# Kernel tuning notes

Hardware: AMD Instinct MI355X
Metric: run time of the kernel (lower is better)

## Reference

```python
import jax, jax.numpy as jnp
import numpy as np

H = 512      # hidden_size
V = 50257    # output_size (vocab)
M = 200      # memory_size
B = 64       # batch


def setup_inputs() -> dict:
    key = jax.random.key(0)
    ks = jax.random.split(key, 24)
    s = 1.0 / np.sqrt(H)
    f32 = jnp.float32
    return {
        "rmn_hidden": jax.random.normal(ks[0], (1, B, H), f32),
        "cell": jax.random.normal(ks[1], (1, B, H), f32),
        "context": jax.random.normal(ks[2], (1, B, H), f32),
        # embedding tables
        "emb": jax.random.normal(ks[3], (V, H), f32) * 0.02,
        "m_emb": jax.random.normal(ks[4], (V, H), f32) * 0.02,
        "c_emb": jax.random.normal(ks[5], (V, H), f32) * 0.02,
        # LSTMCell(2H -> H), torch gate order i, f, g, o
        "lstm_W_ih": jax.random.normal(ks[6], (4 * H, 2 * H), f32) * s,
        "lstm_W_hh": jax.random.normal(ks[7], (4 * H, H), f32) * s,
        "lstm_b_ih": jax.random.normal(ks[8], (4 * H,), f32) * s,
        "lstm_b_hh": jax.random.normal(ks[9], (4 * H,), f32) * s,
        # GRUCell(H -> H), torch gate order r, z, n
        "gru_W_ih": jax.random.normal(ks[10], (3 * H, H), f32) * s,
        "gru_W_hh": jax.random.normal(ks[11], (3 * H, H), f32) * s,
        "gru_b_ih": jax.random.normal(ks[12], (3 * H,), f32) * s,
        "gru_b_hh": jax.random.normal(ks[13], (3 * H,), f32) * s,
        # mb_attn_linear(M -> M)
        "attn_W": jax.random.normal(ks[14], (M, M), f32) * (1.0 / np.sqrt(M)),
        "attn_b": jax.random.normal(ks[15], (M,), f32) * (1.0 / np.sqrt(M)),
        # out Linear(2H -> V)
        "out_W": jax.random.normal(ks[16], (V, 2 * H), f32) * (1.0 / np.sqrt(2 * H)),
        "out_b": jax.random.normal(ks[17], (V,), f32) * (1.0 / np.sqrt(2 * H)),
        # int inputs
        "input_ids": jax.random.randint(ks[18], (1, B), 0, V, jnp.int32),
        "memory_tensor": jax.random.randint(ks[19], (M, B), 0, V, jnp.int32),
        "batch_size": B,
        "memory_size": M,
    }


def reference(rmn_hidden, cell, context, emb, m_emb, c_emb,
              lstm_W_ih, lstm_W_hh, lstm_b_ih, lstm_b_hh,
              gru_W_ih, gru_W_hh, gru_b_ih, gru_b_hh,
              attn_W, attn_b, out_W, out_b,
              input_ids, memory_tensor, batch_size, memory_size):
    sig = jax.nn.sigmoid
    h = rmn_hidden.shape[-1]
    # embedding + relu, concat with context along feature dim
    x = jax.nn.relu(emb[input_ids])                       # (1, B, H)
    ctx = context.reshape(1, batch_size, h)               # (1, B, H)
    xc = jnp.concatenate([x, ctx], axis=2)[0]             # (B, 2H)
    h0, c0 = rmn_hidden[0], cell[0]                       # (B, H)
    # LSTMCell
    gates = xc @ lstm_W_ih.T + lstm_b_ih + h0 @ lstm_W_hh.T + lstm_b_hh
    i, f, g, o = jnp.split(gates, 4, axis=-1)
    c1 = sig(f) * c0 + sig(i) * jnp.tanh(g)
    h1 = sig(o) * jnp.tanh(c1)                            # lstm_hidden (B, H)
    # memory attention
    in_mem = m_emb[memory_tensor]                         # (M, B, H)
    out_mem = c_emb[memory_tensor]                        # (M, B, H)
    attn = jnp.einsum('mbh,bh->bm', in_mem, h1)           # (B, M)
    attn = attn @ attn_W.T + attn_b
    # NOTE: original applies nn.LogSoftmax here (not Softmax) -- faithful.
    attn_dist = jax.nn.log_softmax(attn, axis=-1)         # (B, M)
    memory_context = jnp.einsum('mbh,bm->bh', out_mem, attn_dist)  # (B, H)
    # GRUCell(memory_context, h1)
    gi = memory_context @ gru_W_ih.T + gru_b_ih
    gh = h1 @ gru_W_hh.T + gru_b_hh
    gi_r, gi_z, gi_n = jnp.split(gi, 3, axis=-1)
    gh_r, gh_z, gh_n = jnp.split(gh, 3, axis=-1)
    r = sig(gi_r + gh_r)
    z = sig(gi_z + gh_z)
    n = jnp.tanh(gi_n + r * gh_n)
    mb = (1.0 - z) * n + z * h1                           # (B, H)
    # output projection + log-softmax
    mbc = jnp.concatenate([mb[None], ctx], axis=2)[0]     # (B, 2H)
    output = jax.nn.log_softmax(mbc @ out_W.T + out_b, axis=-1)  # (B, V)
    return (output, h1, c1[None])
```

## Files before the change

### kernel.cpp

```cpp
#include <hip/hip_runtime.h>
#include <math.h>

#define B 64
#define H 512
#define V 50257
#define M 200
#define H2 1024
#define H3 1536
#define H4 2048
#define NB2 1571

typedef short short8 __attribute__((ext_vector_type(8)));
typedef float f32x4 __attribute__((ext_vector_type(4)));

__device__ __forceinline__ float sigf(float x) { return 1.f / (1.f + expf(-x)); }

__device__ __forceinline__ short bf16c(float f) {
  unsigned u = __builtin_bit_cast(unsigned, f);
  unsigned r = u + 0x7fffu + ((u >> 16) & 1u);
  return (short)(r >> 16);
}

__device__ __forceinline__ short8 cvt8(float4 a, float4 b) {
  short8 w;
  w[0] = bf16c(a.x); w[1] = bf16c(a.y); w[2] = bf16c(a.z); w[3] = bf16c(a.w);
  w[4] = bf16c(b.x); w[5] = bf16c(b.y); w[6] = bf16c(b.z); w[7] = bf16c(b.w);
  return w;
}

__global__ __launch_bounds__(256) void k_build_A(
    const float* __restrict__ emb, const float* __restrict__ ctx,
    const float* __restrict__ h0, const int* __restrict__ ids,
    short* __restrict__ A) {
  int k = blockIdx.x * 256 + threadIdx.x;
  int b = blockIdx.y;
  float v;
  if (k < 512) {
    v = emb[(size_t)ids[b] * H + k];
    v = v > 0.f ? v : 0.f;
  } else if (k < 1024) {
    v = ctx[b * H + (k - 512)];
  } else {
    v = h0[b * H + (k - 1024)];
  }
  A[b * H3 + k] = bf16c(v);
}

__global__ __launch_bounds__(256) void k_lstm_gates_mfma(
    const short* __restrict__ A, const float* __restrict__ W_ih,
    const float* __restrict__ W_hh, const float* __restrict__ b_ih,
    const float* __restrict__ b_hh, float* __restrict__ gates) {
  __shared__ float sred[3][64][16];
  const int tid = threadIdx.x;
  const int lane = tid & 63, wid = tid >> 6;
  const int col = lane & 15, g = lane >> 4;
  const int j = blockIdx.x * 16 + col;
  const int kbase = wid * 384;

  f32x4 acc[4];
  #pragma unroll
  for (int t = 0; t < 4; ++t) acc[t] = (f32x4)(0.f);

  #pragma unroll 2
  for (int it = 0; it < 12; ++it) {
    int k0 = kbase + it * 32;
    const float* wp;
    if (k0 < 1024) wp = W_ih + (size_t)j * H2 + k0 + g * 8;
    else           wp = W_hh + (size_t)j * H + (k0 - 1024) + g * 8;
    float4 wa = *(const float4*)wp;
    float4 wb = *(const float4*)(wp + 4);
    short8 bf = cvt8(wa, wb);
    #pragma unroll
    for (int t = 0; t < 4; ++t) {
      short8 af = *(const short8*)(A + (size_t)(col + t * 16) * H3 + k0 + g * 8);
      acc[t] = __builtin_amdgcn_mfma_f32_16x16x32_bf16(af, bf, acc[t], 0, 0, 0);
    }
  }

  if (wid) {
    #pragma unroll
    for (int t = 0; t < 4; ++t)
      #pragma unroll
      for (int r = 0; r < 4; ++r) sred[wid - 1][lane][t * 4 + r] = acc[t][r];
  }
  __syncthreads();
  if (wid == 0) {
    float bias = b_ih[j] + b_hh[j];
    #pragma unroll
    for (int t = 0; t < 4; ++t)
      #pragma unroll
      for (int r = 0; r < 4; ++r) {
        float s = acc[t][r] + sred[0][lane][t * 4 + r] + sred[1][lane][t * 4 + r] +
                  sred[2][lane][t * 4 + r];
        int brow = t * 16 + g * 4 + r;
        gates[brow * H4 + j] = s + bias;
      }
  }
}

__global__ __launch_bounds__(256) void k_lstm_cell(
    const float* __restrict__ gates, const float* __restrict__ c0,
    float* __restrict__ h1, float* __restrict__ c1, short* __restrict__ h1bf) {
  int idx = blockIdx.x * 256 + threadIdx.x;
  int b = idx >> 9, h = idx & 511;
  const float* g = gates + b * H4;
  float gi = g[h], gf = g[H + h], gg = g[2 * H + h], go = g[3 * H + h];
  float c = sigf(gf) * c0[idx] + sigf(gi) * tanhf(gg);
  c1[idx] = c;
  float hv = sigf(go) * tanhf(c);
  h1[idx] = hv;
  h1bf[idx] = bf16c(hv);
}

__global__ __launch_bounds__(256) void k_attn_scores(
    const float* __restrict__ m_emb, const int* __restrict__ mt,
    const float* __restrict__ h1, float* __restrict__ attn) {
  int wave = (blockIdx.x * 256 + threadIdx.x) >> 6;
  int lane = threadIdx.x & 63;
  int m = wave >> 6, b = wave & 63;
  int row = mt[m * B + b];
  const float4* e = (const float4*)(m_emb + (size_t)row * H);
  const float4* hv = (const float4*)(h1 + b * H);
  float4 a0 = e[lane], a1 = e[64 + lane];
  float4 b0 = hv[lane], b1 = hv[64 + lane];
  float acc = a0.x * b0.x + a0.y * b0.y + a0.z * b0.z + a0.w * b0.w +
              a1.x * b1.x + a1.y * b1.y + a1.z * b1.z + a1.w * b1.w;
  for (int off = 32; off > 0; off >>= 1) acc += __shfl_down(acc, off);
  if (lane == 0) attn[b * M + m] = acc;
}

__global__ __launch_bounds__(256) void k_attn_lin_lsm(
    const float* __restrict__ attn, const float* __restrict__ attn_W,
    const float* __restrict__ attn_b, float* __restrict__ attn_d) {
  __shared__ float arow[M];
  __shared__ float vals[256];
  __shared__ float red[256];
  int b = blockIdx.x, tid = threadIdx.x;
  if (tid < M) arow[tid] = attn[b * M + tid];
  __syncthreads();
  float v = -1e30f;
  if (tid < M) {
    const float* w = attn_W + tid * M;
    float a0 = attn_b[tid], a1 = 0.f;
    for (int m = 0; m < M; m += 2) {
      a0 = fmaf(arow[m], w[m], a0);
      a1 = fmaf(arow[m + 1], w[m + 1], a1);
    }
    v = a0 + a1;
  }
  vals[tid] = v;
  red[tid] = v;
  __syncthreads();
  for (int off = 128; off > 0; off >>= 1) {
    if (tid < off) red[tid] = fmaxf(red[tid], red[tid + off]);
    __syncthreads();
  }
  float mx = red[0];
  __syncthreads();
  red[tid] = (tid < M) ? expf(vals[tid] - mx) : 0.f;
  __syncthreads();
  for (int off = 128; off > 0; off >>= 1) {
    if (tid < off) red[tid] += red[tid + off];
    __syncthreads();
  }
  float lse = mx + logf(red[0]);
  if (tid < M) attn_d[b * M + tid] = vals[tid] - lse;
}

__global__ __launch_bounds__(256) void k_mem_ctx_partial(
    const float* __restrict__ c_emb, const int* __restrict__ mt,
    const float* __restrict__ attn_d, float* __restrict__ mcp) {
  int b = blockIdx.x;
  int chunk = blockIdx.y;
  int tid = threadIdx.x;
  __shared__ int rows[50];
  __shared__ float w[50];
  if (tid < 50) {
    int m = chunk * 50 + tid;
    rows[tid] = mt[m * B + b];
    w[tid] = attn_d[b * M + m];
  }
  __syncthreads();
  float acc0 = 0.f, acc1 = 0.f;
  #pragma unroll 5
  for (int i = 0; i < 50; ++i) {
    const float* e = c_emb + (size_t)rows[i] * H;
    acc0 = fmaf(w[i], e[tid], acc0);
    acc1 = fmaf(w[i], e[256 + tid], acc1);
  }
  mcp[(chunk * B + b) * H + tid] = acc0;
  mcp[(chunk * B + b) * H + 256 + tid] = acc1;
}

__global__ __launch_bounds__(256) void k_mem_ctx_reduce(
    const float* __restrict__ mcp, short* __restrict__ mcbf) {
  int idx = blockIdx.x * 256 + threadIdx.x;
  float s = 0.f;
  for (int c = 0; c < 4; ++c) s += mcp[c * (B * H) + idx];
  mcbf[idx] = bf16c(s);
}

__global__ __launch_bounds__(256) void k_gru_gates_mfma(
    const short* __restrict__ mcbf, const short* __restrict__ h1bf,
    const float* __restrict__ W_ih, const float* __restrict__ W_hh,
    const float* __restrict__ b_ih, const float* __restrict__ b_hh,
    float* __restrict__ gi, float* __restrict__ gh) {
  __shared__ float sred[3][64][16];
  const int tid = threadIdx.x;
  const int lane = tid & 63, wid = tid >> 6;
  const int col = lane & 15, g = lane >> 4;
  const int half = blockIdx.x / 96;
  const int j = (blockIdx.x % 96) * 16 + col;
  const short* A = half ? h1bf : mcbf;
  const float* W = half ? W_hh : W_ih;
  const float* bias = half ? b_hh : b_ih;
  float* out = half ? gh : gi;
  const int kbase = wid * 128;

  f32x4 acc[4];
  #pragma unroll
  for (int t = 0; t < 4; ++t) acc[t] = (f32x4)(0.f);

  #pragma unroll
  for (int it = 0; it < 4; ++it) {
    int k0 = kbase + it * 32;
    const float* wp = W + (size_t)j * H + k0 + g * 8;
    float4 wa = *(const float4*)wp;
    float4 wb = *(const float4*)(wp + 4);
    short8 bf = cvt8(wa, wb);
    #pragma unroll
    for (int t = 0; t < 4; ++t) {
      short8 af = *(const short8*)(A + (size_t)(col + t * 16) * H + k0 + g * 8);
      acc[t] = __builtin_amdgcn_mfma_f32_16x16x32_bf16(af, bf, acc[t], 0, 0, 0);
    }
  }

  if (wid) {
    #pragma unroll
    for (int t = 0; t < 4; ++t)
      #pragma unroll
      for (int r = 0; r < 4; ++r) sred[wid - 1][lane][t * 4 + r] = acc[t][r];
  }
  __syncthreads();
  if (wid == 0) {
    float bv = bias[j];
    #pragma unroll
    for (int t = 0; t < 4; ++t)
      #pragma unroll
      for (int r = 0; r < 4; ++r) {
        float s = acc[t][r] + sred[0][lane][t * 4 + r] + sred[1][lane][t * 4 + r] +
                  sred[2][lane][t * 4 + r];
        int brow = t * 16 + g * 4 + r;
        out[brow * H3 + j] = s + bv;
      }
  }
}

__global__ __launch_bounds__(256) void k_gru_combine(
    const float* __restrict__ gi, const float* __restrict__ gh,
    const float* __restrict__ h1, const float* __restrict__ ctx,
    short* __restrict__ Abf) {
  int idx = blockIdx.x * 256 + threadIdx.x;
  int b = idx >> 9, h = idx & 511;
  const float* gib = gi + b * H3;
  const float* ghb = gh + b * H3;
  float r = sigf(gib[h] + ghb[h]);
  float z = sigf(gib[H + h] + ghb[H + h]);
  float n = tanhf(gib[2 * H + h] + r * ghb[2 * H + h]);
  float mb = (1.f - z) * n + z * h1[idx];
  Abf[b * H2 + h] = bf16c(mb);
  Abf[b * H2 + H + h] = bf16c(ctx[idx]);
}

__global__ __launch_bounds__(256) void k_out_gemm_mfma(
    const short* __restrict__ Abf, const float* __restrict__ W,
    const float* __restrict__ bias, float* __restrict__ out,
    float* __restrict__ pm, float* __restrict__ ps) {
  __shared__ short8 Wl[512];
  __shared__ float spm[4][32];
  __shared__ float sps[4][32];
  const int tid = threadIdx.x;
  const int lane = tid & 63, wid = tid >> 6;
  const int v0 = blockIdx.x * 32;

  const int sr = tid >> 3, sj = tid & 7;
  const int sidx = sr * 8 + (sj ^ (sr & 7));
  int vr = v0 + sr; if (vr >= V) vr = V - 1;
  const float* wsrc = W + (size_t)vr * H2 + sj * 8;

  const int col = lane & 15, g = lane >> 4;
  const int ct = wid & 1, bh = wid >> 1;
  const int wrow = ct * 16 + col;
  const short* a0p = Abf + (size_t)(bh * 32 + col) * H2 + g * 8;
  const short* a1p = a0p + 16 * H2;

  f32x4 acc0 = (f32x4)(0.f), acc1 = (f32x4)(0.f);

  {
    float4 wa = *(const float4*)(wsrc);
    float4 wb = *(const float4*)(wsrc + 4);
    Wl[sidx] = cvt8(wa, wb);
  }
  __syncthreads();

  int cur = 0;
  for (int kt = 0; kt < 16; ++kt) {
    float4 nwa, nwb;
    if (kt < 15) {
      nwa = *(const float4*)(wsrc + (kt + 1) * 64);
      nwb = *(const float4*)(wsrc + (kt + 1) * 64 + 4);
    }
    {
      const short8* Wb = Wl + cur * 256;
      #pragma unroll
      for (int kw = 0; kw < 2; ++kw) {
        int c = kw * 4 + g;
        short8 bf  = Wb[wrow * 8 + (c ^ (wrow & 7))];
        short8 af0 = *(const short8*)(a0p + kt * 64 + kw * 32);
        short8 af1 = *(const short8*)(a1p + kt * 64 + kw * 32);
        acc0 = __builtin_amdgcn_mfma_f32_16x16x32_bf16(af0, bf, acc0, 0, 0, 0);
        acc1 = __builtin_amdgcn_mfma_f32_16x16x32_bf16(af1, bf, acc1, 0, 0, 0);
      }
    }
    if (kt < 15) {
      Wl[(cur ^ 1) * 256 + sidx] = cvt8(nwa, nwb);
      __syncthreads();
      cur ^= 1;
    }
  }

  const int v = v0 + ct * 16 + col;
  const float bv = (v < V) ? bias[v] : 0.f;
  #pragma unroll
  for (int ai = 0; ai < 2; ++ai) {
    f32x4 a = ai ? acc1 : acc0;
    #pragma unroll
    for (int r = 0; r < 4; ++r) {
      int b = bh * 32 + ai * 16 + g * 4 + r;
      float x = a[r] + bv;
      if (v < V) out[(size_t)b * V + v] = x;
      float xm = (v < V) ? x : -1e30f;
      float mx = xm;
      #pragma unroll
      for (int off = 1; off < 16; off <<= 1) mx = fmaxf(mx, __shfl_xor(mx, off));
      float e = (v < V) ? expf(xm - mx) : 0.f;
      #pragma unroll
      for (int off = 1; off < 16; off <<= 1) e += __shfl_xor(e, off);
      if (col == 0) {
        spm[wid][ai * 16 + g * 4 + r] = mx;
        sps[wid][ai * 16 + g * 4 + r] = e;
      }
    }
  }
  __syncthreads();
  if (tid < 64) {
    int b = tid;
    int w0 = (b >> 5) * 2;
    int bl = b & 31;
    float m1 = spm[w0][bl],     s1 = sps[w0][bl];
    float m2 = spm[w0 + 1][bl], s2 = sps[w0 + 1][bl];
    float nm = fmaxf(m1, m2);
    float s = s1 * expf(m1 - nm) + s2 * expf(m2 - nm);
    pm[(size_t)b * NB2 + blockIdx.x] = nm;
    ps[(size_t)b * NB2 + blockIdx.x] = s;
  }
}

__global__ __launch_bounds__(256) void k_lsm_finalize(
    const float* __restrict__ pm, const float* __restrict__ ps,
    float* __restrict__ lse) {
  int b = blockIdx.x, tid = threadIdx.x;
  float m = -1e30f, s = 0.f;
  for (int gq = tid; gq < NB2; gq += 256) {
    float m2 = pm[(size_t)b * NB2 + gq], s2 = ps[(size_t)b * NB2 + gq];
    float nm = fmaxf(m, m2);
    s = s * expf(m - nm) + s2 * expf(m2 - nm);
    m = nm;
  }
  __shared__ float sm[256], ss[256];
  sm[tid] = m; ss[tid] = s;
  __syncthreads();
  for (int off = 128; off > 0; off >>= 1) {
    if (tid < off) {
      float m1 = sm[tid], s1 = ss[tid];
      float m2 = sm[tid + off], s2 = ss[tid + off];
      float nm = fmaxf(m1, m2);
      sm[tid] = nm;
      ss[tid] = s1 * expf(m1 - nm) + s2 * expf(m2 - nm);
    }
    __syncthreads();
  }
  if (tid == 0) lse[b] = sm[0] + logf(ss[0]);
}

__global__ __launch_bounds__(256) void k_lsm_apply(
    float* __restrict__ out, const float* __restrict__ lse) {
  int b = blockIdx.y, tid = threadIdx.x;
  float l = lse[b];
  int v = blockIdx.x * 1024 + tid * 4;
  float* row = out + (size_t)b * V;
  if (v + 3 < V) {
    float4 x = *(const float4*)(row + v);
    x.x -= l; x.y -= l; x.z -= l; x.w -= l;
    *(float4*)(row + v) = x;
  } else {
    for (int i = 0; i < 4 && v + i < V; ++i) row[v + i] -= l;
  }
}

extern "C" void kernel_launch(void* const* d_in, const int* in_sizes, int n_in,
                              void* d_out, int out_size, void* d_ws, size_t ws_size,
                              hipStream_t stream) {
  const float* h0    = (const float*)d_in[0];
  const float* c0    = (const float*)d_in[1];
  const float* ctx   = (const float*)d_in[2];
  const float* emb   = (const float*)d_in[3];
  const float* m_emb = (const float*)d_in[4];
  const float* c_emb = (const float*)d_in[5];
  const float* lWih  = (const float*)d_in[6];
  const float* lWhh  = (const float*)d_in[7];
  const float* lbih  = (const float*)d_in[8];
  const float* lbhh  = (const float*)d_in[9];
  const float* gWih  = (const float*)d_in[10];
  const float* gWhh  = (const float*)d_in[11];
  const float* gbih  = (const float*)d_in[12];
  const float* gbhh  = (const float*)d_in[13];
  const float* aW    = (const float*)d_in[14];
  const float* ab    = (const float*)d_in[15];
  const float* oW    = (const float*)d_in[16];
  const float* ob    = (const float*)d_in[17];
  const int* ids     = (const int*)d_in[18];
  const int* mt      = (const int*)d_in[19];

  float* out = (float*)d_out;
  float* h1  = out + (size_t)B * V;
  float* c1  = h1 + B * H;

  float* ws    = (float*)d_ws;
  short* Albf  = (short*)ws;
  float* gates = ws + 49152;
  short* h1bf  = (short*)(gates + B * H4);
  float* attn  = gates + B * H4 + 16384;
  float* attnd = attn + B * M;
  float* mcp   = attnd + B * M;
  short* mcbf  = (short*)(mcp + 4 * B * H);
  float* gi    = mcp + 4 * B * H + 16384;
  float* gh    = gi + B * H3;
  short* Abf   = (short*)(gh + B * H3);
  float* pm    = gh + B * H3 + 32768;
  float* ps    = pm + (size_t)B * NB2;
  float* lse   = ps + (size_t)B * NB2;

  dim3 g1(6, B);
  k_build_A<<<g1, 256, 0, stream>>>(emb, ctx, h0, ids, Albf);
  k_lstm_gates_mfma<<<128, 256, 0, stream>>>(Albf, lWih, lWhh, lbih, lbhh, gates);
  k_lstm_cell<<<(B * H) / 256, 256, 0, stream>>>(gates, c0, h1, c1, h1bf);
  k_attn_scores<<<(M * B) / 4, 256, 0, stream>>>(m_emb, mt, h1, attn);
  k_attn_lin_lsm<<<B, 256, 0, stream>>>(attn, aW, ab, attnd);
  dim3 g6(B, 4);
  k_mem_ctx_partial<<<g6, 256, 0, stream>>>(c_emb, mt, attnd, mcp);
  k_mem_ctx_reduce<<<(B * H) / 256, 256, 0, stream>>>(mcp, mcbf);
  k_gru_gates_mfma<<<192, 256, 0, stream>>>(mcbf, h1bf, gWih, gWhh, gbih, gbhh, gi, gh);
  k_gru_combine<<<(B * H) / 256, 256, 0, stream>>>(gi, gh, h1, ctx, Abf);
  k_out_gemm_mfma<<<NB2, 256, 0, stream>>>(Abf, oW, ob, out, pm, ps);
  k_lsm_finalize<<<B, 256, 0, stream>>>(pm, ps, lse);
  dim3 g11(50, B);
  k_lsm_apply<<<g11, 256, 0, stream>>>(out, lse);
}
```

Baseline: 137.3 us.

## Widen output GEMM tile to 64 vocab rows and stage activations in LDS

The output projection kernel now computes 64 vocab rows per block instead of 32, halving the block count. Each wave computes a 32x32 tile with four MFMA accumulators, so every A and W fragment is reused twice. The bf16 activation matrix is also staged through swizzled, double-buffered shared memory rather than read from global memory by each wave. This cuts repeated activation loads and the number of partial log-softmax entries, at the cost of more LDS and registers per block and fewer blocks to spread across CUs.

```diff
diff --git a/kernel.cpp b/kernel.cpp
--- a/kernel.cpp
+++ b/kernel.cpp
@@ -8,7 +8,7 @@
 #define H2 1024
 #define H3 1536
 #define H4 2048
-#define NB2 1571
+#define NB 786
 
 typedef short short8 __attribute__((ext_vector_type(8)));
 typedef float f32x4 __attribute__((ext_vector_type(4)));
@@ -276,78 +276,110 @@
     const short* __restrict__ Abf, const float* __restrict__ W,
     const float* __restrict__ bias, float* __restrict__ out,
     float* __restrict__ pm, float* __restrict__ ps) {
-  __shared__ short8 Wl[512];
+  __shared__ short8 Wl[1024];
+  __shared__ short8 Al[1024];
   __shared__ float spm[4][32];
   __shared__ float sps[4][32];
   const int tid = threadIdx.x;
   const int lane = tid & 63, wid = tid >> 6;
-  const int v0 = blockIdx.x * 32;
-
-  const int sr = tid >> 3, sj = tid & 7;
-  const int sidx = sr * 8 + (sj ^ (sr & 7));
+  const int v0 = blockIdx.x * 64;
+
+  const int sr = tid >> 2, sj = tid & 3;
+  const int sx = sr & 7;
+  const int sidx0 = sr * 8 + ((2 * sj) ^ sx);
+  const int sidx1 = sr * 8 + ((2 * sj + 1) ^ sx);
   int vr = v0 + sr; if (vr >= V) vr = V - 1;
-  const float* wsrc = W + (size_t)vr * H2 + sj * 8;
+  const float* wsrc = W + (size_t)vr * H2 + sj * 16;
+  const short* asrc = Abf + (size_t)sr * H2 + sj * 16;
 
   const int col = lane & 15, g = lane >> 4;
-  const int ct = wid & 1, bh = wid >> 1;
-  const int wrow = ct * 16 + col;
-  const short* a0p = Abf + (size_t)(bh * 32 + col) * H2 + g * 8;
-  const short* a1p = a0p + 16 * H2;
-
-  f32x4 acc0 = (f32x4)(0.f), acc1 = (f32x4)(0.f);
+  const int vhalf = wid & 1, bhalf = wid >> 1;
+  const int wr0 = vhalf * 32 + col, wr1 = wr0 + 16;
+  const int ar0 = bhalf * 32 + col, ar1 = ar0 + 16;
+
+  f32x4 acc00 = (f32x4)(0.f), acc01 = (f32x4)(0.f);
+  f32x4 acc10 = (f32x4)(0.f), acc11 = (f32x4)(0.f);
 
   {
-    float4 wa = *(const float4*)(wsrc);
-    float4 wb = *(const float4*)(wsrc + 4);
-    Wl[sidx] = cvt8(wa, wb);
+    float4 wa0 = *(const float4*)(wsrc);
+    float4 wb0 = *(const float4*)(wsrc + 4);
+    float4 wa1 = *(const float4*)(wsrc + 8);
+    float4 wb1 = *(const float4*)(wsrc + 12);
+    short8 av0 = *(const short8*)(asrc);
+    short8 av1 = *(const short8*)(asrc + 8);
+    Wl[sidx0] = cvt8(wa0, wb0);
+    Wl[sidx1] = cvt8(wa1, wb1);
+    Al[sidx0] = av0;
+    Al[sidx1] = av1;
   }
   __syncthreads();
 
   int cur = 0;
   for (int kt = 0; kt < 16; ++kt) {
-    float4 nwa, nwb;
+    float4 nwa0, nwb0, nwa1, nwb1;
+    short8 nav0, nav1;
     if (kt < 15) {
-      nwa = *(const float4*)(wsrc + (kt + 1) * 64);
-      nwb = *(const float4*)(wsrc + (kt + 1) * 64 + 4);
+      const float* wn = wsrc + (kt + 1) * 64;
+      nwa0 = *(const float4*)(wn);
+      nwb0 = *(const float4*)(wn + 4);
+      nwa1 = *(const float4*)(wn + 8);
+      nwb1 = *(const float4*)(wn + 12);
+      const short* an = asrc + (kt + 1) * 64;
+      nav0 = *(const short8*)(an);
+      nav1 = *(const short8*)(an + 8);
     }
     {
-      const short8* Wb = Wl + cur * 256;
+      const short8* Wb = Wl + cur * 512;
+      const short8* Ab = Al + cur * 512;
       #pragma unroll
       for (int kw = 0; kw < 2; ++kw) {
         int c = kw * 4 + g;
-        short8 bf  = Wb[wrow * 8 + (c ^ (wrow & 7))];
-        short8 af0 = *(const short8*)(a0p + kt * 64 + kw * 32);
-        short8 af1 = *(const short8*)(a1p + kt * 64 + kw * 32);
-        acc0 = __builtin_amdgcn_mfma_f32_16x16x32_bf16(af0, bf, acc0, 0, 0, 0);
-        acc1 = __builtin_amdgcn_mfma_f32_16x16x32_bf16(af1, bf, acc1, 0, 0, 0);
+        short8 bf0 = Wb[wr0 * 8 + (c ^ (wr0 & 7))];
+        short8 bf1 = Wb[wr1 * 8 + (c ^ (wr1 & 7))];
+        short8 af0 = Ab[ar0 * 8 + (c ^ (ar0 & 7))];
+        short8 af1 = Ab[ar1 * 8 + (c ^ (ar1 & 7))];
+        acc00 = __builtin_amdgcn_mfma_f32_16x16x32_bf16(af0, bf0, acc00, 0, 0, 0);
+        acc01 = __builtin_amdgcn_mfma_f32_16x16x32_bf16(af0, bf1, acc01, 0, 0, 0);
+        acc10 = __builtin_amdgcn_mfma_f32_16x16x32_bf16(af1, bf0, acc10, 0, 0, 0);
+        acc11 = __builtin_amdgcn_mfma_f32_16x16x32_bf16(af1, bf1, acc11, 0, 0, 0);
       }
     }
     if (kt < 15) {
-      Wl[(cur ^ 1) * 256 + sidx] = cvt8(nwa, nwb);
+      Wl[(cur ^ 1) * 512 + sidx0] = cvt8(nwa0, nwb0);
+      Wl[(cur ^ 1) * 512 + sidx1] = cvt8(nwa1, nwb1);
+      Al[(cur ^ 1) * 512 + sidx0] = nav0;
+      Al[(cur ^ 1) * 512 + sidx1] = nav1;
       __syncthreads();
       cur ^= 1;
     }
   }
 
-  const int v = v0 + ct * 16 + col;
-  const float bv = (v < V) ? bias[v] : 0.f;
   #pragma unroll
   for (int ai = 0; ai < 2; ++ai) {
-    f32x4 a = ai ? acc1 : acc0;
     #pragma unroll
     for (int r = 0; r < 4; ++r) {
-      int b = bh * 32 + ai * 16 + g * 4 + r;
-      float x = a[r] + bv;
-      if (v < V) out[(size_t)b * V + v] = x;
-      float xm = (v < V) ? x : -1e30f;
-      float mx = xm;
+      int b = bhalf * 32 + ai * 16 + g * 4 + r;
+      float mx[2], ee[2];
       #pragma unroll
-      for (int off = 1; off < 16; off <<= 1) mx = fmaxf(mx, __shfl_xor(mx, off));
-      float e = (v < V) ? expf(xm - mx) : 0.f;
-      #pragma unroll
-      for (int off = 1; off < 16; off <<= 1) e += __shfl_xor(e, off);
+      for (int u = 0; u < 2; ++u) {
+        int v = v0 + vhalf * 32 + u * 16 + col;
+        f32x4 a = ai ? (u ? acc11 : acc10) : (u ? acc01 : acc00);
+        float bv = (v < V) ? bias[v] : 0.f;
+        float x = a[r] + bv;
+        if (v < V) out[(size_t)b * V + v] = x;
+        float xm = (v < V) ? x : -1e30f;
+        float m = xm;
+        #pragma unroll
+        for (int off = 1; off < 16; off <<= 1) m = fmaxf(m, __shfl_xor(m, off));
+        float e = (v < V) ? expf(xm - m) : 0.f;
+        #pragma unroll
+        for (int off = 1; off < 16; off <<= 1) e += __shfl_xor(e, off);
+        mx[u] = m; ee[u] = e;
+      }
+      float m = fmaxf(mx[0], mx[1]);
+      float e = ee[0] * expf(mx[0] - m) + ee[1] * expf(mx[1] - m);
       if (col == 0) {
-        spm[wid][ai * 16 + g * 4 + r] = mx;
+        spm[wid][ai * 16 + g * 4 + r] = m;
         sps[wid][ai * 16 + g * 4 + r] = e;
       }
     }
@@ -361,8 +393,8 @@
     float m2 = spm[w0 + 1][bl], s2 = sps[w0 + 1][bl];
     float nm = fmaxf(m1, m2);
     float s = s1 * expf(m1 - nm) + s2 * expf(m2 - nm);
-    pm[(size_t)b * NB2 + blockIdx.x] = nm;
-    ps[(size_t)b * NB2 + blockIdx.x] = s;
+    pm[(size_t)b * NB + blockIdx.x] = nm;
+    ps[(size_t)b * NB + blockIdx.x] = s;
   }
 }
 
@@ -371,8 +403,8 @@
     float* __restrict__ lse) {
   int b = blockIdx.x, tid = threadIdx.x;
   float m = -1e30f, s = 0.f;
-  for (int gq = tid; gq < NB2; gq += 256) {
-    float m2 = pm[(size_t)b * NB2 + gq], s2 = ps[(size_t)b * NB2 + gq];
+  for (int gq = tid; gq < NB; gq += 256) {
+    float m2 = pm[(size_t)b * NB + gq], s2 = ps[(size_t)b * NB + gq];
     float nm = fmaxf(m, m2);
     s = s * expf(m - nm) + s2 * expf(m2 - nm);
     m = nm;
@@ -448,8 +480,8 @@
   float* gh    = gi + B * H3;
   short* Abf   = (short*)(gh + B * H3);
   float* pm    = gh + B * H3 + 32768;
-  float* ps    = pm + (size_t)B * NB2;
-  float* lse   = ps + (size_t)B * NB2;
+  float* ps    = pm + (size_t)B * NB;
+  float* lse   = ps + (size_t)B * NB;
 
   dim3 g1(6, B);
   k_build_A<<<g1, 256, 0, stream>>>(emb, ctx, h0, ids, Albf);
@@ -462,7 +494,7 @@
   k_mem_ctx_reduce<<<(B * H) / 256, 256, 0, stream>>>(mcp, mcbf);
   k_gru_gates_mfma<<<192, 256, 0, stream>>>(mcbf, h1bf, gWih, gWhh, gbih, gbhh, gi, gh);
   k_gru_combine<<<(B * H) / 256, 256, 0, stream>>>(gi, gh, h1, ctx, Abf);
-  k_out_gemm_mfma<<<NB2, 256, 0, stream>>>(Abf, oW, ob, out, pm, ps);
+  k_out_gemm_mfma<<<NB, 256, 0, stream>>>(Abf, oW, ob, out, pm, ps);
   k_lsm_finalize<<<B, 256, 0, stream>>>(pm, ps, lse);
   dim3 g11(50, B);
   k_lsm_apply<<<g11, 256, 0, stream>>>(out, lse);
```

After: 117.4 us. 14.5% less time.
